# Kernel optimization log

Measured on AMD Instinct MI355X. Metric: run time of the kernel, lower is better.

Reference implementation:

```python
import jax, jax.numpy as jnp
import numpy as np
from jax.ops import segment_sum

N = 100000   # total nodes
M = 50000    # propagated subset size (len(index))
E = 600000   # edges over the subset graph
D = 128      # embedding_size
EPS = 1e-8
N_LAYERS = 3  # self.LayerNums


def setup_inputs() -> dict:
    key = jax.random.key(0)
    ks = jax.random.split(key, 12)
    features = jax.random.normal(ks[0], (N, D), dtype=jnp.float32)
    index = jnp.arange(M, dtype=jnp.int64)  # subset of nodes that get propagated
    edge_row = jax.random.randint(ks[1], (E,), 0, M, dtype=jnp.int64)
    edge_col = jax.random.randint(ks[2], (E,), 0, M, dtype=jnp.int64)
    edge_val = jax.random.uniform(ks[3], (E,), dtype=jnp.float32)
    # MLP prediction weights: D -> D//2 -> D//4 -> D//6 -> 1 (last no bias)
    def xavier(k, fan_in, fan_out):
        lim = jnp.sqrt(6.0 / (fan_in + fan_out)).astype(jnp.float32)
        return jax.random.uniform(k, (fan_in, fan_out), jnp.float32, -lim, lim)
    W1 = xavier(ks[4], D, D // 2); b1 = jnp.zeros((D // 2,), jnp.float32)
    W2 = xavier(ks[5], D // 2, D // 4); b2 = jnp.zeros((D // 4,), jnp.float32)
    W3 = xavier(ks[6], D // 4, D // 6); b3 = jnp.zeros((D // 6,), jnp.float32)
    W4 = xavier(ks[7], D // 6, 1)
    return {"features": features, "index": index, "edge_row": edge_row,
            "edge_col": edge_col, "edge_val": edge_val,
            "W1": W1, "b1": b1, "W2": W2, "b2": b2, "W3": W3, "b3": b3, "W4": W4}


def _gcn_layer(features, index, row, col, val):
    # symmetric normalization: d = rowsum(A)+eps; A' = d^-1/2 A d^-1/2
    deg = segment_sum(val, row, num_segments=M)
    d_inv_sqrt = jax.lax.rsqrt(deg + EPS)
    nval = val * d_inv_sqrt[row] * d_inv_sqrt[col]
    sub = features[index]                      # [M, D] subset_features
    msg = sub[col] * nval[:, None]             # [E, D]
    out = segment_sum(msg, row, num_segments=M)  # spmm -> [M, D]
    # new_features[index] = out; untouched rows keep original features
    return features.at[index].set(out)


def reference(features, index, edge_row, edge_col, edge_val,
              W1, b1, W2, b2, W3, b3, W4):
    x = features
    for _ in range(N_LAYERS):
        x = _gcn_layer(x, index, edge_row, edge_col, edge_val)
    # MLP prediction head (eval mode: dropout off), LeakyReLU slope 0.01
    h = jax.nn.leaky_relu(x @ W1 + b1, 0.01)
    h = jax.nn.leaky_relu(h @ W2 + b2, 0.01)
    h = jax.nn.leaky_relu(h @ W3 + b3, 0.01)
    return jax.nn.sigmoid(h @ W4)              # [N, 1]
```

## Files before the change

### kernel.cpp

```cpp
#include <hip/hip_runtime.h>
#include <math.h>

#define NN 100000
#define MM 50000
#define EE 600000
#define DD 128
#define NB 196
#define NNP 100096

typedef short bf16x8 __attribute__((ext_vector_type(8)));
typedef float f32x4 __attribute__((ext_vector_type(4)));

__device__ __forceinline__ float bl(unsigned u) { return __uint_as_float(u << 16); }
__device__ __forceinline__ float bh(unsigned u) { return __uint_as_float(u & 0xFFFF0000u); }
__device__ __forceinline__ unsigned rne(float f) {
    unsigned u = __float_as_uint(f);
    return (u + 0x7FFFu + ((u >> 16) & 1u)) >> 16;
}
__device__ __forceinline__ unsigned pk2(float a, float b) { return rne(a) | (rne(b) << 16); }

__device__ __forceinline__ void fmab8(float v, uint4 u, float* a) {
    a[0] = fmaf(v, bl(u.x), a[0]); a[1] = fmaf(v, bh(u.x), a[1]);
    a[2] = fmaf(v, bl(u.y), a[2]); a[3] = fmaf(v, bh(u.y), a[3]);
    a[4] = fmaf(v, bl(u.z), a[4]); a[5] = fmaf(v, bh(u.z), a[5]);
    a[6] = fmaf(v, bl(u.w), a[6]); a[7] = fmaf(v, bh(u.w), a[7]);
}

__device__ __forceinline__ void fma21(float h, const float* wrow, float* a) {
    #pragma unroll
    for (int j = 0; j < 21; ++j) a[j] = fmaf(h, wrow[j], a[j]);
}

__global__ void deg_count_kernel(const int* __restrict__ row, const float* __restrict__ val,
                                 unsigned long long* __restrict__ dcpack,
                                 int* __restrict__ slot, int* __restrict__ invidx) {
    int e = blockIdx.x * 256 + threadIdx.x;
    if (e < NN) invidx[e] = -1;
    if (e < EE) {
        int r = row[e];
        unsigned long long add = (1ULL << 44) | (unsigned long long)(val[e] * 4294967296.0f);
        unsigned long long old = atomicAdd(&dcpack[r], add);
        slot[e] = (int)(old >> 44);
    }
}

__global__ void fused_setup_kernel(const unsigned long long* __restrict__ dcpack,
                                   float* __restrict__ dis,
                                   const int* __restrict__ index, int* __restrict__ invidx,
                                   int* __restrict__ cnt, int* __restrict__ partial,
                                   int* __restrict__ bsum) {
    __shared__ int ws[4];
    int tid = threadIdx.x, lane = tid & 63, w = tid >> 6;
    int i = blockIdx.x * 256 + tid;
    int v = 0;
    if (i < MM) {
        unsigned long long pkv = dcpack[i];
        v = (int)(pkv >> 44);
        float dsum = (float)(pkv & ((1ULL << 44) - 1)) * (1.0f / 4294967296.0f);
        dis[i] = rsqrtf(dsum + 1e-8f);
        invidx[index[i]] = i;
        cnt[i] = v;
    }
    int x = v;
    #pragma unroll
    for (int off = 1; off < 64; off <<= 1) {
        int t = __shfl_up(x, off, 64);
        if (lane >= off) x += t;
    }
    if (lane == 63) ws[w] = x;
    __syncthreads();
    int add = 0;
    for (int q = 0; q < w; ++q) add += ws[q];
    x += add;
    if (i < MM) partial[i] = x;
    if (tid == 255) bsum[blockIdx.x] = x;
}

__global__ void scanB_kernel(const int* __restrict__ bsum, int* __restrict__ boff) {
    int lane = threadIdx.x;
    int carry = 0;
    for (int base = 0; base < NB; base += 64) {
        int v = (base + lane < NB) ? bsum[base + lane] : 0;
        int x = v;
        #pragma unroll
        for (int off = 1; off < 64; off <<= 1) {
            int t = __shfl_up(x, off, 64);
            if (lane >= off) x += t;
        }
        if (base + lane < NB) boff[base + lane] = carry + x - v;
        carry += __shfl(x, 63);
    }
}

__global__ void scanC_kernel(const int* __restrict__ partial, const int* __restrict__ cnt,
                             const int* __restrict__ boff, int* __restrict__ rowptr) {
    int i = blockIdx.x * 256 + threadIdx.x;
    if (i < MM) rowptr[i] = partial[i] - cnt[i] + boff[i >> 8];
    if (i == 0) rowptr[MM] = EE;
}

__global__ void scatter_kernel(const int* __restrict__ row, const int* __restrict__ col,
                               const float* __restrict__ val, const float* __restrict__ dis,
                               const int* __restrict__ rowptr, const int* __restrict__ slot,
                               int* __restrict__ col_s, float* __restrict__ val_s) {
    int e = blockIdx.x * 256 + threadIdx.x;
    if (e < EE) {
        int r = row[e], c = col[e];
        int pos = rowptr[r] + slot[e];
        col_s[pos] = c;
        val_s[pos] = val[e] * dis[r] * dis[c];
    }
}

__global__ void cvt_kernel(const float* __restrict__ feat, const int* __restrict__ index,
                           const int* __restrict__ invidx,
                           unsigned* __restrict__ X0b, unsigned* __restrict__ Xfull,
                           const float* __restrict__ W1, const float* __restrict__ W2,
                           unsigned* __restrict__ W1b, unsigned* __restrict__ W2b) {
    int i = blockIdx.x * 256 + threadIdx.x;
    int n = i >> 6, u = i & 63;
    if (n < NN && invidx[n] < 0) {
        float2 f = ((const float2*)feat)[(size_t)n * 64 + u];
        Xfull[(size_t)n * 64 + u] = pk2(f.x, f.y);
    }
    if (i < MM * 64) {
        int idx = index[n];
        float2 f = ((const float2*)feat)[(size_t)idx * 64 + u];
        X0b[i] = pk2(f.x, f.y);
    }
    if (i < 4096) {
        int j = i >> 6, kp = i & 63;
        W1b[i] = pk2(W1[(2 * kp) * 64 + j], W1[(2 * kp + 1) * 64 + j]);
    } else if (i < 5120) {
        int t = i - 4096;
        int j = t >> 5, kp = t & 31;
        W2b[t] = pk2(W2[(2 * kp) * 32 + j], W2[(2 * kp + 1) * 32 + j]);
    }
}

__global__ __launch_bounds__(256) void spmm_kernel(
    const int* __restrict__ rowptr, const int* __restrict__ cols,
    const float* __restrict__ vals, const unsigned short* __restrict__ X,
    unsigned short* __restrict__ Y, const int* __restrict__ remap) {
    int lane = threadIdx.x & 63;
    int wid = threadIdx.x >> 6;
    int g = lane >> 4, sub = lane & 15;
    int r = blockIdx.x * 16 + wid * 4 + g;
    bool valid = (r < MM);
    int rc = valid ? r : (MM - 1);
    int s = rowptr[rc], e = rowptr[rc + 1];
    const uint4* __restrict__ X4 = (const uint4*)X;
    float a[8] = {0.f, 0.f, 0.f, 0.f, 0.f, 0.f, 0.f, 0.f};
    for (int base = s; base < e; base += 16) {
        int cnt = min(16, e - base);
        int c = 0; float v = 0.f;
        if (sub < cnt) { c = cols[base + sub]; v = vals[base + sub]; }
        int j = 0;
        for (; j + 4 <= cnt; j += 4) {
            int c0 = __shfl(c, g * 16 + j);     float v0 = __shfl(v, g * 16 + j);
            int c1 = __shfl(c, g * 16 + j + 1); float v1 = __shfl(v, g * 16 + j + 1);
            int c2 = __shfl(c, g * 16 + j + 2); float v2 = __shfl(v, g * 16 + j + 2);
            int c3 = __shfl(c, g * 16 + j + 3); float v3 = __shfl(v, g * 16 + j + 3);
            uint4 u0 = X4[(size_t)c0 * 16 + sub];
            uint4 u1 = X4[(size_t)c1 * 16 + sub];
            uint4 u2 = X4[(size_t)c2 * 16 + sub];
            uint4 u3 = X4[(size_t)c3 * 16 + sub];
            fmab8(v0, u0, a);
            fmab8(v1, u1, a);
            fmab8(v2, u2, a);
            fmab8(v3, u3, a);
        }
        for (; j < cnt; ++j) {
            int cc = __shfl(c, g * 16 + j); float vv = __shfl(v, g * 16 + j);
            uint4 u0 = X4[(size_t)cc * 16 + sub];
            fmab8(vv, u0, a);
        }
    }
    if (valid) {
        int dst = remap ? remap[rc] : rc;
        uint4 o;
        o.x = pk2(a[0], a[1]); o.y = pk2(a[2], a[3]);
        o.z = pk2(a[4], a[5]); o.w = pk2(a[6], a[7]);
        ((uint4*)Y)[(size_t)dst * 16 + sub] = o;
    }
}

__global__ __launch_bounds__(256) void mlp_kernel(
    const unsigned* __restrict__ Xfull,
    const unsigned* __restrict__ W1b, const float* __restrict__ b1,
    const unsigned* __restrict__ W2b, const float* __restrict__ b2,
    const float* __restrict__ W3, const float* __restrict__ b3,
    const float* __restrict__ W4, float* __restrict__ out) {
    __shared__ float hls[4 * 1088];
    int tid = threadIdx.x;
    int lane = tid & 63, w = tid >> 6;
    int p = lane & 15, q = lane >> 4;
    float* hw = hls + w * 1088;
    int nb = blockIdx.x * 64;
    int node = nb + w * 16 + p;

    bf16x8 af[4];
    #pragma unroll
    for (int kc = 0; kc < 4; ++kc) {
        uint4 u = *(const uint4*)(Xfull + (size_t)node * 64 + kc * 16 + q * 4);
        af[kc] = *(const bf16x8*)&u;
    }
    f32x4 acc[4];
    #pragma unroll
    for (int jt = 0; jt < 4; ++jt) {
        float bv = b1[jt * 16 + p];
        acc[jt][0] = bv; acc[jt][1] = bv; acc[jt][2] = bv; acc[jt][3] = bv;
    }
    #pragma unroll
    for (int jt = 0; jt < 4; ++jt) {
        #pragma unroll
        for (int kc = 0; kc < 4; ++kc) {
            uint4 u = *(const uint4*)(W1b + (jt * 16 + p) * 64 + kc * 16 + q * 4);
            bf16x8 bf = *(const bf16x8*)&u;
            acc[jt] = __builtin_amdgcn_mfma_f32_16x16x32_bf16(af[kc], bf, acc[jt], 0, 0, 0);
        }
    }
    #pragma unroll
    for (int jt = 0; jt < 4; ++jt) {
        #pragma unroll
        for (int r = 0; r < 4; ++r) {
            float v = acc[jt][r];
            v = v > 0.f ? v : 0.01f * v;
            hw[(q * 4 + r) * 68 + jt * 16 + p] = v;
        }
    }
    bf16x8 a2f[2];
    #pragma unroll
    for (int kc = 0; kc < 2; ++kc) {
        const float* hp = hw + p * 68 + kc * 32 + q * 8;
        f32x4 v0 = *(const f32x4*)hp;
        f32x4 v1 = *(const f32x4*)(hp + 4);
        uint4 uu = make_uint4(pk2(v0[0], v0[1]), pk2(v0[2], v0[3]),
                              pk2(v1[0], v1[1]), pk2(v1[2], v1[3]));
        a2f[kc] = *(const bf16x8*)&uu;
    }
    f32x4 acc2[2];
    #pragma unroll
    for (int jt = 0; jt < 2; ++jt) {
        float bv = b2[jt * 16 + p];
        acc2[jt][0] = bv; acc2[jt][1] = bv; acc2[jt][2] = bv; acc2[jt][3] = bv;
        #pragma unroll
        for (int kc = 0; kc < 2; ++kc) {
            uint4 u = *(const uint4*)(W2b + (jt * 16 + p) * 32 + kc * 16 + q * 4);
            bf16x8 bf = *(const bf16x8*)&u;
            acc2[jt] = __builtin_amdgcn_mfma_f32_16x16x32_bf16(a2f[kc], bf, acc2[jt], 0, 0, 0);
        }
    }
    #pragma unroll
    for (int jt = 0; jt < 2; ++jt) {
        #pragma unroll
        for (int r = 0; r < 4; ++r) {
            float v = acc2[jt][r];
            v = v > 0.f ? v : 0.01f * v;
            hw[(q * 4 + r) * 36 + jt * 16 + p] = v;
        }
    }
    float a3[21];
    #pragma unroll
    for (int j = 0; j < 21; ++j) a3[j] = b3[j];
    #pragma unroll 4
    for (int k = 0; k < 32; ++k) {
        float hk = hw[p * 36 + k];
        fma21(hk, W3 + k * 21, a3);
    }
    float s = 0.f;
    #pragma unroll
    for (int j = 0; j < 21; ++j) {
        float vj = a3[j] > 0.f ? a3[j] : 0.01f * a3[j];
        s = fmaf(vj, W4[j], s);
    }
    if (q == 0) {
        int n = nb + w * 16 + p;
        if (n < NN) out[n] = 1.f / (1.f + expf(-s));
    }
}

extern "C" void kernel_launch(void* const* d_in, const int* in_sizes, int n_in,
                              void* d_out, int out_size, void* d_ws, size_t ws_size,
                              hipStream_t stream) {
    const float* feat = (const float*)d_in[0];
    const int*   index = (const int*)d_in[1];
    const int*   erow = (const int*)d_in[2];
    const int*   ecol = (const int*)d_in[3];
    const float* evalp = (const float*)d_in[4];
    const float* W1 = (const float*)d_in[5];
    const float* b1 = (const float*)d_in[6];
    const float* W2 = (const float*)d_in[7];
    const float* b2 = (const float*)d_in[8];
    const float* W3 = (const float*)d_in[9];
    const float* b3 = (const float*)d_in[10];
    const float* W4 = (const float*)d_in[11];
    float* out = (float*)d_out;

    char* ws = (char*)d_ws;
    size_t off = 0;
    auto alloc = [&](size_t bytes) -> void* {
        void* p = ws + off;
        off += (bytes + 255) & ~(size_t)255;
        return p;
    };
    unsigned long long* dcpack = (unsigned long long*)alloc((size_t)MM * 8);
    float* dis     = (float*)alloc((size_t)MM * 4);
    int*   cnt     = (int*)  alloc((size_t)MM * 4);
    int*   rowptr  = (int*)  alloc((size_t)(MM + 1) * 4);
    int*   partial = (int*)  alloc((size_t)MM * 4);
    int*   bsum    = (int*)  alloc((size_t)NB * 4);
    int*   boff    = (int*)  alloc((size_t)NB * 4);
    int*   slot    = (int*)  alloc((size_t)EE * 4);
    int*   col_s   = (int*)  alloc((size_t)EE * 4);
    float* val_s   = (float*)alloc((size_t)EE * 4);
    int*   invidx  = (int*)  alloc((size_t)NN * 4);
    unsigned* W1b  = (unsigned*)alloc(4096 * 4);
    unsigned* W2b  = (unsigned*)alloc(1024 * 4);
    unsigned*       X0b   = (unsigned*)      alloc((size_t)MM * DD * 2);
    unsigned short* Xa    = (unsigned short*)alloc((size_t)MM * DD * 2);
    unsigned short* Xb    = (unsigned short*)alloc((size_t)MM * DD * 2);
    unsigned*       Xfull = (unsigned*)      alloc((size_t)NNP * DD * 2);

    hipMemsetAsync(dcpack, 0, (size_t)MM * 8, stream);

    deg_count_kernel<<<(EE + 255) / 256, 256, 0, stream>>>(erow, evalp, dcpack, slot, invidx);
    fused_setup_kernel<<<NB, 256, 0, stream>>>(dcpack, dis, index, invidx, cnt, partial, bsum);
    scanB_kernel<<<1, 64, 0, stream>>>(bsum, boff);
    scanC_kernel<<<(MM + 255) / 256, 256, 0, stream>>>(partial, cnt, boff, rowptr);
    scatter_kernel<<<(EE + 255) / 256, 256, 0, stream>>>(erow, ecol, evalp, dis,
                                                         rowptr, slot, col_s, val_s);
    cvt_kernel<<<(NN * 64 + 255) / 256, 256, 0, stream>>>(feat, index, invidx, X0b, Xfull,
                                                          W1, W2, W1b, W2b);

    spmm_kernel<<<(MM + 15) / 16, 256, 0, stream>>>(rowptr, col_s, val_s,
                                                    (const unsigned short*)X0b, Xa, nullptr);
    spmm_kernel<<<(MM + 15) / 16, 256, 0, stream>>>(rowptr, col_s, val_s, Xa, Xb, nullptr);
    spmm_kernel<<<(MM + 15) / 16, 256, 0, stream>>>(rowptr, col_s, val_s, Xb,
                                                    (unsigned short*)Xfull, index);

    mlp_kernel<<<(NNP + 63) / 64, 256, 0, stream>>>(Xfull, W1b, b1, W2b, b2,
                                                    W3, b3, W4, out);
}
```

Baseline: 265.5 us.

## Drop X0b gather copy by reading first layer through remapped columns

Removes the inverse-index map and the separate gathered subset copy X0b. Instead, the scatter step stores a second column array pre-mapped through index, so the first SpMM reads the full converted feature table directly. Row-pointer computation is folded into the scatter kernel, which removes the scanC launch. The SpMM inner loop gains an 8-way unrolled gather stage for more loads in flight. The cost is an extra 600K-int column array, and the third layer writing into Xfull while the first layer read from it relies on stream ordering.

```diff
diff --git a/kernel.cpp b/kernel.cpp
--- a/kernel.cpp
+++ b/kernel.cpp
@@ -33,9 +33,8 @@
 
 __global__ void deg_count_kernel(const int* __restrict__ row, const float* __restrict__ val,
                                  unsigned long long* __restrict__ dcpack,
-                                 int* __restrict__ slot, int* __restrict__ invidx) {
+                                 int* __restrict__ slot) {
     int e = blockIdx.x * 256 + threadIdx.x;
-    if (e < NN) invidx[e] = -1;
     if (e < EE) {
         int r = row[e];
         unsigned long long add = (1ULL << 44) | (unsigned long long)(val[e] * 4294967296.0f);
@@ -46,7 +45,6 @@
 
 __global__ void fused_setup_kernel(const unsigned long long* __restrict__ dcpack,
                                    float* __restrict__ dis,
-                                   const int* __restrict__ index, int* __restrict__ invidx,
                                    int* __restrict__ cnt, int* __restrict__ partial,
                                    int* __restrict__ bsum) {
     __shared__ int ws[4];
@@ -58,7 +56,6 @@
         v = (int)(pkv >> 44);
         float dsum = (float)(pkv & ((1ULL << 44) - 1)) * (1.0f / 4294967296.0f);
         dis[i] = rsqrtf(dsum + 1e-8f);
-        invidx[index[i]] = i;
         cnt[i] = v;
     }
     int x = v;
@@ -92,41 +89,36 @@
     }
 }
 
-__global__ void scanC_kernel(const int* __restrict__ partial, const int* __restrict__ cnt,
-                             const int* __restrict__ boff, int* __restrict__ rowptr) {
-    int i = blockIdx.x * 256 + threadIdx.x;
-    if (i < MM) rowptr[i] = partial[i] - cnt[i] + boff[i >> 8];
-    if (i == 0) rowptr[MM] = EE;
-}
-
 __global__ void scatter_kernel(const int* __restrict__ row, const int* __restrict__ col,
                                const float* __restrict__ val, const float* __restrict__ dis,
-                               const int* __restrict__ rowptr, const int* __restrict__ slot,
-                               int* __restrict__ col_s, float* __restrict__ val_s) {
+                               const int* __restrict__ index,
+                               const int* __restrict__ partial, const int* __restrict__ cnt,
+                               const int* __restrict__ boff, const int* __restrict__ slot,
+                               int* __restrict__ rowptr,
+                               int* __restrict__ col_s, int* __restrict__ colf_s,
+                               float* __restrict__ val_s) {
     int e = blockIdx.x * 256 + threadIdx.x;
+    if (e < MM) rowptr[e] = partial[e] - cnt[e] + boff[e >> 8];
+    if (e == MM) rowptr[MM] = EE;
     if (e < EE) {
         int r = row[e], c = col[e];
-        int pos = rowptr[r] + slot[e];
+        int pos = (partial[r] - cnt[r] + boff[r >> 8]) + slot[e];
         col_s[pos] = c;
+        colf_s[pos] = index[c];
         val_s[pos] = val[e] * dis[r] * dis[c];
     }
 }
 
-__global__ void cvt_kernel(const float* __restrict__ feat, const int* __restrict__ index,
-                           const int* __restrict__ invidx,
-                           unsigned* __restrict__ X0b, unsigned* __restrict__ Xfull,
-                           const float* __restrict__ W1, const float* __restrict__ W2,
-                           unsigned* __restrict__ W1b, unsigned* __restrict__ W2b) {
+__global__ void prep_kernel(const float* __restrict__ feat, unsigned* __restrict__ Xfull,
+                            const float* __restrict__ W1, const float* __restrict__ W2,
+                            unsigned* __restrict__ W1b, unsigned* __restrict__ W2b) {
     int i = blockIdx.x * 256 + threadIdx.x;
     int n = i >> 6, u = i & 63;
-    if (n < NN && invidx[n] < 0) {
+    if (n < NN) {
         float2 f = ((const float2*)feat)[(size_t)n * 64 + u];
-        Xfull[(size_t)n * 64 + u] = pk2(f.x, f.y);
-    }
-    if (i < MM * 64) {
-        int idx = index[n];
-        float2 f = ((const float2*)feat)[(size_t)idx * 64 + u];
-        X0b[i] = pk2(f.x, f.y);
+        Xfull[i] = pk2(f.x, f.y);
+    } else if (n < NNP) {
+        Xfull[i] = 0;
     }
     if (i < 4096) {
         int j = i >> 6, kp = i & 63;
@@ -156,6 +148,28 @@
         int c = 0; float v = 0.f;
         if (sub < cnt) { c = cols[base + sub]; v = vals[base + sub]; }
         int j = 0;
+        for (; j + 8 <= cnt; j += 8) {
+            int c0 = __shfl(c, g * 16 + j);     float v0 = __shfl(v, g * 16 + j);
+            int c1 = __shfl(c, g * 16 + j + 1); float v1 = __shfl(v, g * 16 + j + 1);
+            int c2 = __shfl(c, g * 16 + j + 2); float v2 = __shfl(v, g * 16 + j + 2);
+            int c3 = __shfl(c, g * 16 + j + 3); float v3 = __shfl(v, g * 16 + j + 3);
+            int c4 = __shfl(c, g * 16 + j + 4); float v4 = __shfl(v, g * 16 + j + 4);
+            int c5 = __shfl(c, g * 16 + j + 5); float v5 = __shfl(v, g * 16 + j + 5);
+            int c6 = __shfl(c, g * 16 + j + 6); float v6 = __shfl(v, g * 16 + j + 6);
+            int c7 = __shfl(c, g * 16 + j + 7); float v7 = __shfl(v, g * 16 + j + 7);
+            uint4 u0 = X4[(size_t)c0 * 16 + sub];
+            uint4 u1 = X4[(size_t)c1 * 16 + sub];
+            uint4 u2 = X4[(size_t)c2 * 16 + sub];
+            uint4 u3 = X4[(size_t)c3 * 16 + sub];
+            uint4 u4 = X4[(size_t)c4 * 16 + sub];
+            uint4 u5 = X4[(size_t)c5 * 16 + sub];
+            uint4 u6 = X4[(size_t)c6 * 16 + sub];
+            uint4 u7 = X4[(size_t)c7 * 16 + sub];
+            fmab8(v0, u0, a); fmab8(v1, u1, a);
+            fmab8(v2, u2, a); fmab8(v3, u3, a);
+            fmab8(v4, u4, a); fmab8(v5, u5, a);
+            fmab8(v6, u6, a); fmab8(v7, u7, a);
+        }
         for (; j + 4 <= cnt; j += 4) {
             int c0 = __shfl(c, g * 16 + j);     float v0 = __shfl(v, g * 16 + j);
             int c1 = __shfl(c, g * 16 + j + 1); float v1 = __shfl(v, g * 16 + j + 1);
@@ -165,10 +179,8 @@
             uint4 u1 = X4[(size_t)c1 * 16 + sub];
             uint4 u2 = X4[(size_t)c2 * 16 + sub];
             uint4 u3 = X4[(size_t)c3 * 16 + sub];
-            fmab8(v0, u0, a);
-            fmab8(v1, u1, a);
-            fmab8(v2, u2, a);
-            fmab8(v3, u3, a);
+            fmab8(v0, u0, a); fmab8(v1, u1, a);
+            fmab8(v2, u2, a); fmab8(v3, u3, a);
         }
         for (; j < cnt; ++j) {
             int cc = __shfl(c, g * 16 + j); float vv = __shfl(v, g * 16 + j);
@@ -313,32 +325,29 @@
     int*   boff    = (int*)  alloc((size_t)NB * 4);
     int*   slot    = (int*)  alloc((size_t)EE * 4);
     int*   col_s   = (int*)  alloc((size_t)EE * 4);
+    int*   colf_s  = (int*)  alloc((size_t)EE * 4);
     float* val_s   = (float*)alloc((size_t)EE * 4);
-    int*   invidx  = (int*)  alloc((size_t)NN * 4);
     unsigned* W1b  = (unsigned*)alloc(4096 * 4);
     unsigned* W2b  = (unsigned*)alloc(1024 * 4);
-    unsigned*       X0b   = (unsigned*)      alloc((size_t)MM * DD * 2);
     unsigned short* Xa    = (unsigned short*)alloc((size_t)MM * DD * 2);
     unsigned short* Xb    = (unsigned short*)alloc((size_t)MM * DD * 2);
     unsigned*       Xfull = (unsigned*)      alloc((size_t)NNP * DD * 2);
 
     hipMemsetAsync(dcpack, 0, (size_t)MM * 8, stream);
 
-    deg_count_kernel<<<(EE + 255) / 256, 256, 0, stream>>>(erow, evalp, dcpack, slot, invidx);
-    fused_setup_kernel<<<NB, 256, 0, stream>>>(dcpack, dis, index, invidx, cnt, partial, bsum);
+    deg_count_kernel<<<(EE + 255) / 256, 256, 0, stream>>>(erow, evalp, dcpack, slot);
+    fused_setup_kernel<<<NB, 256, 0, stream>>>(dcpack, dis, cnt, partial, bsum);
     scanB_kernel<<<1, 64, 0, stream>>>(bsum, boff);
-    scanC_kernel<<<(MM + 255) / 256, 256, 0, stream>>>(partial, cnt, boff, rowptr);
-    scatter_kernel<<<(EE + 255) / 256, 256, 0, stream>>>(erow, ecol, evalp, dis,
-                                                         rowptr, slot, col_s, val_s);
-    cvt_kernel<<<(NN * 64 + 255) / 256, 256, 0, stream>>>(feat, index, invidx, X0b, Xfull,
-                                                          W1, W2, W1b, W2b);
-
-    spmm_kernel<<<(MM + 15) / 16, 256, 0, stream>>>(rowptr, col_s, val_s,
-                                                    (const unsigned short*)X0b, Xa, nullptr);
+    scatter_kernel<<<(EE + 255) / 256, 256, 0, stream>>>(erow, ecol, evalp, dis, index,
+                                                         partial, cnt, boff, slot, rowptr,
+                                                         col_s, colf_s, val_s);
+    prep_kernel<<<(NNP * 64) / 256, 256, 0, stream>>>(feat, Xfull, W1, W2, W1b, W2b);
+
+    spmm_kernel<<<(MM + 15) / 16, 256, 0, stream>>>(rowptr, colf_s, val_s,
+                                                    (const unsigned short*)Xfull, Xa, nullptr);
     spmm_kernel<<<(MM + 15) / 16, 256, 0, stream>>>(rowptr, col_s, val_s, Xa, Xb, nullptr);
     spmm_kernel<<<(MM + 15) / 16, 256, 0, stream>>>(rowptr, col_s, val_s, Xb,
                                                     (unsigned short*)Xfull, index);
 
-    mlp_kernel<<<(NNP + 63) / 64, 256, 0, stream>>>(Xfull, W1b, b1, W2b, b2,
-                                                    W3, b3, W4, out);
-}
+    mlp_kernel<<<NNP / 64, 256, 0, stream>>>(Xfull, W1b, b1, W2b, b2, W3, b3, W4, out);
+}
```

Result: slower. 272.6 us (+2.7%).
